# Kernel optimization log

Measured on AMD Instinct MI355X. Metric: run time of the kernel, lower is better.

## Reference

```python
import jax, jax.numpy as jnp
import numpy as np

B, S = 512, 256          # batch, seq_len
C, H = 8, 16             # num_cells, expert hidden size
M = 20                   # memory_size (hard-coded in module)
NT = C * H               # num_trajectories = 128
ENC_IN = M * (NT + 1)    # 20*129 = 2580, memory_encode input dim
A_H = 16                 # agent LSTM hidden


def setup_inputs() -> dict:
    key = jax.random.key(0)
    ks = jax.random.split(key, 20)
    r = lambda i, shape: 0.1 * jax.random.normal(ks[i], shape, dtype=jnp.float32)
    return {
        "x": jax.random.normal(ks[0], (B, S, 1), dtype=jnp.float32),
        "pred0": jax.random.uniform(ks[1], (B, 1), dtype=jnp.float32),
        "gate0": jax.nn.softmax(jax.random.uniform(ks[2], (B, C), dtype=jnp.float32), axis=1),
        # experts: C parallel LSTM cells (input 1, hidden H) + per-cell scalar head
        "W_ih": r(3, (C, 4 * H, 1)), "W_hh": r(4, (C, 4 * H, H)),
        "b_ih": r(5, (C, 4 * H)), "b_hh": r(6, (C, 4 * H)),
        "W_o": r(7, (C, H)), "b_o": r(8, (C,)),
        # memory_encode: Linear(2580,64) ReLU Linear(64,16) ReLU
        "W1": r(9, (64, ENC_IN)), "b1": r(10, (64,)),
        "W2": r(11, (16, 64)), "b2": r(12, (16,)),
        # gate_linear: Linear(16, C) + softmax
        "Wg": r(13, (C, 16)), "bg": r(14, (C,)),
        # agent: 2 stacked LSTM cells (16 -> 16)
        "Wa_ih": r(15, (2, 4 * A_H, A_H)), "Wa_hh": r(16, (2, 4 * A_H, A_H)),
        "ba_ih": r(17, (2, 4 * A_H)), "ba_hh": r(18, (2, 4 * A_H)),
    }


def _cell(z, c):
    # PyTorch LSTMCell gate order: i, f, g, o
    i, f, g, o = jnp.split(z, 4, axis=-1)
    c2 = jax.nn.sigmoid(f) * c + jax.nn.sigmoid(i) * jnp.tanh(g)
    return jax.nn.sigmoid(o) * jnp.tanh(c2), c2


def reference(x, pred0, gate0, W_ih, W_hh, b_ih, b_hh, W_o, b_o,
              W1, b1, W2, b2, Wg, bg, Wa_ih, Wa_hh, ba_ih, ba_hh):
    mem0 = jnp.zeros((B, M, NT + 1), jnp.float32).at[:, :, -1].set(0.5)
    eh0 = jnp.zeros((B, H), jnp.float32)   # combined expert h (shared across cells)
    a0 = jnp.zeros((2, B, A_H), jnp.float32)

    def step(carry, x_t):
        mem, eh, ec, pred, gate_state, ah, ac = carry
        error = x_t - pred                                        # [B,1]
        # experts: C LSTM cells, all reading the shared combined state
        z = (jnp.einsum('bf,cgf->bcg', x_t, W_ih)
             + jnp.einsum('bh,cgh->bcg', eh, W_hh)
             + b_ih + b_hh)                                       # [B,C,4H]
        nh, nc = _cell(z, ec[:, None, :])                          # [B,C,H]
        o = jnp.einsum('bch,ch->bc', nh, W_o) + b_o               # [B,C]
        # memory_step: matmul(mstep, mem) shifts rows down by 1, row 0 <- w
        w = jnp.concatenate([nh.reshape(B, -1), error], axis=1)   # [B,NT+1]
        mem = jnp.concatenate([w[:, None, :], mem[:, :-1, :]], axis=1)
        # memory_encode MLP
        e1 = jax.nn.relu(mem.reshape(B, -1) @ W1.T + b1)
        ai = jax.nn.relu(e1 @ W2.T + b2)                           # [B,16]
        # agent: 2 stacked LSTM cells
        ah_l, ac_l, inp_l = [], [], ai
        for l in range(2):
            zl = inp_l @ Wa_ih[l].T + ba_ih[l] + ah[l] @ Wa_hh[l].T + ba_hh[l]
            hl, cl = _cell(zl, ac[l])
            ah_l.append(hl); ac_l.append(cl)
            inp_l = hl
        ah2, ac2 = jnp.stack(ah_l), jnp.stack(ac_l)
        gate = jax.nn.softmax(inp_l @ Wg.T + bg, axis=1)           # [B,C]
        # theta = clip(2.5 * mean|mem[:, :10, -1]|, 0, 1)  (relu(t)-relu(t-1))
        theta = jnp.clip(jnp.mean(jnp.abs(mem[:, :10, -1]), axis=1) * 2.5, 0.0, 1.0)[:, None]
        gate = gate * theta + gate_state * (1.0 - theta)
        eh2 = jnp.einsum('bc,bch->bh', gate, nh)                   # bmm(gate, h)
        ec2 = jnp.einsum('bc,bch->bh', gate, nc)
        pred2 = jnp.einsum('bc,bc->b', gate, o)[:, None]           # [B,1]
        return (mem, eh2, ec2, pred2, gate, ah2, ac2), pred2

    xs = jnp.swapaxes(x, 0, 1)  # [S,B,1]
    _, preds = jax.lax.scan(step, (mem0, eh0, eh0, pred0, gate0, a0, a0), xs)
    return jnp.swapaxes(preds, 0, 1)  # [B,S,1]
```

## Files before the change

### kernel.cpp

```cpp
#include <hip/hip_runtime.h>
#include <math.h>

#define S_LEN 256
#define NCELL 8
#define HID 16
#define MEM 20
#define NB 4
#define NTHR 512
#define RSTR 2592

typedef _Float16 v8h __attribute__((ext_vector_type(8)));
typedef float v4f __attribute__((ext_vector_type(4)));

__device__ __forceinline__ float sigm(float v) { return 1.0f / (1.0f + __expf(-v)); }
__device__ __forceinline__ float tanh_f(float v) { return 1.0f - 2.0f / (__expf(2.0f * v) + 1.0f); }
__device__ __forceinline__ float dot4(float4 a, float4 b) {
    return fmaf(a.x, b.x, fmaf(a.y, b.y, fmaf(a.z, b.z, a.w * b.w)));
}
__device__ __forceinline__ v4f mfma16(v8h a, v8h b, v4f c) {
    return __builtin_amdgcn_mfma_f32_16x16x32_f16(a, b, c, 0, 0, 0);
}

#define RING(b, s, k) ringH[(b) * RSTR + (s) * 128 + (k)]

__global__ __launch_bounds__(256)
void prep_w1(const float* __restrict__ W1, _Float16* __restrict__ W1F) {
    int idx = blockIdx.x * 256 + threadIdx.x;
    if (idx < MEM * 4 * 4 * 64 * 8) {
        int e = idx & 7;
        int lane = (idx >> 3) & 63;
        int jt = (idx >> 9) & 3;
        int t = idx >> 11;
        int m = t >> 2, kc = t & 3;
        int j = jt * 16 + (lane & 15);
        int k = kc * 32 + (lane >> 4) * 8 + e;
        W1F[idx] = (_Float16)W1[j * 2580 + m * 129 + k];
    }
}

#define E1P(BB, V) { \
    V = b1_l[lane] \
      + red[par][1][BB][lane] + red[par][2][BB][lane] + red[par][3][BB][lane] \
      + red[par][4][BB][lane] + red[par][5][BB][lane] + red[par][6][BB][lane] \
      + red[par][7][BB][lane]; }

#define E1F(BB, V) { \
    V += errdotS[BB][lane] \
       + red0[0][BB][lane] + red0[1][BB][lane] + red0[2][BB][lane] + red0[3][BB][lane]; \
    e1S[BB][lane] = fmaxf(V, 0.f); }

__global__ __attribute__((amdgpu_flat_work_group_size(NTHR, NTHR)))
void mmoe_kernel(const float* __restrict__ x, const float* __restrict__ pred0,
                 const float* __restrict__ gate0,
                 const float* __restrict__ W_ih, const float* __restrict__ W_hh,
                 const float* __restrict__ b_ih, const float* __restrict__ b_hh,
                 const float* __restrict__ W_o, const float* __restrict__ b_o,
                 const float* __restrict__ W1, const float* __restrict__ b1,
                 const float* __restrict__ W2, const float* __restrict__ b2,
                 const float* __restrict__ Wg, const float* __restrict__ bg,
                 const float* __restrict__ Wa_ih, const float* __restrict__ Wa_hh,
                 const float* __restrict__ ba_ih, const float* __restrict__ ba_hh,
                 const _Float16* __restrict__ W1F,
                 float* __restrict__ out)
{
    __shared__ __align__(16) _Float16 ringH[NB * RSTR];
    __shared__ __align__(16) _Float16 W10F_l[8192];
    __shared__ float errS[NB][MEM];
    __shared__ __align__(16) float Whh_l[512 * 20];
    __shared__ float Wih_l[512], bias_l[512];
    __shared__ __align__(16) float WaI[2][64 * 20], WaH[2][64 * 20];
    __shared__ float ba_l[2][64];
    __shared__ __align__(16) float W2_l[16 * 68];
    __shared__ float b2_l[16];
    __shared__ __align__(16) float Wg_l[8][16], Wo_l[8][16];
    __shared__ float bg_l[8], bo_l[8];
    __shared__ float Werr_l[MEM * 64];
    __shared__ float b1_l[64];
    __shared__ float xS[NB][S_LEN];
    __shared__ __align__(16) float ehS[NB][HID], ecS[NB][HID];
    __shared__ __align__(16) float nhS[NB][NCELL][HID], ncS[NB][NCELL][HID];
    __shared__ float oS[NB][NCELL], predS[NB], gateS[NB][NCELL];
    __shared__ __align__(16) float ahS[2][NB][HID], acS[2][NB][HID];
    __shared__ __align__(16) float e1S[NB][64], aiS[NB][HID];
    __shared__ __align__(16) float glog[NB][8];
    __shared__ __align__(16) float red[2][8][NB][64];
    __shared__ __align__(16) float red0[4][NB][64];
    __shared__ float errdotS[NB][64];
    __shared__ float thS[NB];

    const int tid = threadIdx.x;
    const int b0 = blockIdx.x * NB;
    const int lane = tid & 63, wv = tid >> 6;
    const int quad = lane >> 4, nn = lane & 15, bb4 = nn & 3;

    for (int i = tid; i < 512 * 16; i += NTHR) { int g = i >> 4, q = i & 15; Whh_l[g * 20 + q] = W_hh[i]; }
    for (int i = tid; i < 512; i += NTHR) { Wih_l[i] = W_ih[i]; bias_l[i] = b_ih[i] + b_hh[i]; }
    for (int i = tid; i < 2048; i += NTHR) {
        int l = i >> 10, r = i & 1023, g = r >> 4, q = r & 15;
        WaI[l][g * 20 + q] = Wa_ih[i]; WaH[l][g * 20 + q] = Wa_hh[i];
    }
    for (int i = tid; i < 128; i += NTHR) { int l = i >> 6, g = i & 63; ba_l[l][g] = ba_ih[i] + ba_hh[i]; }
    for (int i = tid; i < 1024; i += NTHR) { int r = i >> 6, q = i & 63; W2_l[r * 68 + q] = W2[i]; }
    for (int i = tid; i < 1280; i += NTHR) { int m = i >> 6, j = i & 63; Werr_l[i] = W1[j * 2580 + m * 129 + 128]; }
    for (int i = tid; i < 8192; i += NTHR) W10F_l[i] = W1F[i];
    if (tid < 64) b1_l[tid] = b1[tid];
    if (tid < 16) b2_l[tid] = b2[tid];
    if (tid < 128) { int c = tid >> 4, h = tid & 15; Wg_l[c][h] = Wg[tid]; Wo_l[c][h] = W_o[tid]; }
    if (tid < 8) { bg_l[tid] = bg[tid]; bo_l[tid] = b_o[tid]; }
    for (int i = tid; i < NB * S_LEN; i += NTHR) { int b = i >> 8, s = i & 255; xS[b][s] = x[(b0 + b) * S_LEN + s]; }
    for (int i = tid; i < NB * RSTR; i += NTHR) ringH[i] = (_Float16)0.0f;
    for (int i = tid; i < 2 * 8 * NB * 64; i += NTHR) ((float*)red)[i] = 0.0f;
    if (tid < NB * MEM) { int b = tid / MEM, m = tid % MEM; errS[b][m] = 0.5f; }
    if (tid < NB * HID) {
        int b = tid >> 4, h = tid & 15;
        ehS[b][h] = 0.f; ecS[b][h] = 0.f;
        ahS[0][b][h] = 0.f; ahS[1][b][h] = 0.f;
        acS[0][b][h] = 0.f; acS[1][b][h] = 0.f;
    }
    if (tid < NB) predS[tid] = pred0[b0 + tid];
    if (tid < NB * NCELL) { int b = tid >> 3, c = tid & 7; gateS[b][c] = gate0[(b0 + b) * NCELL + c]; }
    __syncthreads();

    const v8h* Wb = (const v8h*)W1F;
    const v8h* WL = (const v8h*)W10F_l;

    int head = 0;
    #pragma unroll 1
    for (int t = 0; t < S_LEN; ++t) {
        head = (head == 0) ? (MEM - 1) : (head - 1);
        const int par = t & 1, np = par ^ 1;
        float v0, v1, v2, v3;

        {
            int b = tid >> 7, c = (tid >> 4) & 7, h = tid & 15;
            float xv = xS[b][t];
            const float4* ep = (const float4*)&ehS[b][0];
            float4 e0 = ep[0], e1v = ep[1], e2 = ep[2], e3 = ep[3];
            float zg[4];
            #pragma unroll
            for (int gi = 0; gi < 4; ++gi) {
                int g = c * 64 + gi * 16 + h;
                const float* wr = &Whh_l[g * 20];
                float z = bias_l[g] + xv * Wih_l[g];
                z += dot4(e0, *(const float4*)&wr[0]) + dot4(e1v, *(const float4*)&wr[4])
                   + dot4(e2, *(const float4*)&wr[8]) + dot4(e3, *(const float4*)&wr[12]);
                zg[gi] = z;
            }
            float cc = ecS[b][h];
            float c2 = sigm(zg[1]) * cc + sigm(zg[0]) * tanh_f(zg[2]);
            float hv = sigm(zg[3]) * tanh_f(c2);
            nhS[b][c][h] = hv; ncS[b][c][h] = c2;
            RING(b, head, c * 16 + h) = (_Float16)hv;
            if (tid < NB) errS[tid][head] = xS[tid][t] - predS[tid];
        }
        __syncthreads();

        {
            int kc = wv >> 1, jt0 = (wv & 1) * 2;
            v8h bfrag = *(const v8h*)&RING(bb4, head, kc * 32 + quad * 8);
            v8h a0 = WL[(kc * 4 + jt0) * 64 + lane];
            v8h a1 = WL[(kc * 4 + jt0 + 1) * 64 + lane];
            v4f z = {0.f, 0.f, 0.f, 0.f};
            v4f c0 = mfma16(a0, bfrag, z);
            v4f c1 = mfma16(a1, bfrag, z);
            if (nn < 4) {
                *(v4f*)&red0[kc][nn][jt0 * 16 + quad * 4] = c0;
                *(v4f*)&red0[kc][nn][(jt0 + 1) * 16 + quad * 4] = c1;
            }
            if (wv == 0) {
                E1P(0, v0) E1P(1, v1) E1P(2, v2) E1P(3, v3)
            } else if (wv == 1) {
                if (lane < 32) {
                    int bb = lane >> 3, c = lane & 7;
                    const float4* np_ = (const float4*)&nhS[bb][c][0];
                    const float4* wp = (const float4*)&Wo_l[c][0];
                    float s = bo_l[c];
                    #pragma unroll
                    for (int q4 = 0; q4 < 4; ++q4) s += dot4(np_[q4], wp[q4]);
                    oS[bb][c] = s;
                }
            } else if (wv == 2) {
                if (lane < NB) {
                    float th = 0.f;
                    #pragma unroll
                    for (int m = 0; m < 10; ++m) {
                        int sl = head + m; if (sl >= MEM) sl -= MEM;
                        th += fabsf(errS[lane][sl]);
                    }
                    th *= 0.25f;
                    thS[lane] = fminf(fmaxf(th, 0.f), 1.f);
                }
            } else if (wv >= 3 && wv < 7) {
                int bb = wv - 3;
                float s = 0.f;
                int sl = head;
                #pragma unroll
                for (int m = 0; m < MEM; ++m) {
                    s = fmaf(Werr_l[m * 64 + lane], errS[bb][sl], s);
                    ++sl; if (sl >= MEM) sl = 0;
                }
                errdotS[bb][lane] = s;
            }
        }
        __syncthreads();

        if (wv >= 1) {
            int kt = (wv - 1) * 11;
            int ktEnd = kt + 11; if (ktEnd > 76) ktEnd = 76;
            v4f c0 = {0.f,0.f,0.f,0.f}, c1 = {0.f,0.f,0.f,0.f};
            v4f c2 = {0.f,0.f,0.f,0.f}, c3 = {0.f,0.f,0.f,0.f};
            size_t t0 = (size_t)(4 + kt) * 256 + lane;
            v8h aA0 = Wb[t0], aA1 = Wb[t0 + 64], aA2 = Wb[t0 + 128], aA3 = Wb[t0 + 192];
            int m0 = 1 + (kt >> 2), kc0 = kt & 3;
            int s0 = head + m0 - 1; if (s0 >= MEM) s0 -= MEM;
            v8h aB = *(const v8h*)&RING(bb4, s0, kc0 * 32 + quad * 8);
            size_t t1 = t0 + 256;
            v8h bA0 = Wb[t1], bA1 = Wb[t1 + 64], bA2 = Wb[t1 + 128], bA3 = Wb[t1 + 192];
            int k1 = kt + 1, m1 = 1 + (k1 >> 2), kc1 = k1 & 3;
            int s1 = head + m1 - 1; if (s1 >= MEM) s1 -= MEM;
            v8h bB = *(const v8h*)&RING(bb4, s1, kc1 * 32 + quad * 8);
            #pragma unroll 1
            for (int i = kt; i < ktEnd; ++i) {
                v8h uA0 = aA0, uA1 = aA1, uA2 = aA2, uA3 = aA3, uB = aB;
                aA0 = bA0; aA1 = bA1; aA2 = bA2; aA3 = bA3; aB = bB;
                int kn = i + 2;
                if (kn < ktEnd) {
                    size_t tn = (size_t)(4 + kn) * 256 + lane;
                    bA0 = Wb[tn]; bA1 = Wb[tn + 64]; bA2 = Wb[tn + 128]; bA3 = Wb[tn + 192];
                    int mn = 1 + (kn >> 2), kcn = kn & 3;
                    int sn = head + mn - 1; if (sn >= MEM) sn -= MEM;
                    bB = *(const v8h*)&RING(bb4, sn, kcn * 32 + quad * 8);
                }
                c0 = mfma16(uA0, uB, c0);
                c1 = mfma16(uA1, uB, c1);
                c2 = mfma16(uA2, uB, c2);
                c3 = mfma16(uA3, uB, c3);
            }
            if (nn < 4) {
                *(v4f*)&red[np][wv][nn][ 0 + quad * 4] = c0;
                *(v4f*)&red[np][wv][nn][16 + quad * 4] = c1;
                *(v4f*)&red[np][wv][nn][32 + quad * 4] = c2;
                *(v4f*)&red[np][wv][nn][48 + quad * 4] = c3;
            }
        } else {
            E1F(0, v0) E1F(1, v1) E1F(2, v2) E1F(3, v3)
            const int j = lane;
            {
                int bb = j >> 4, i = j & 15;
                const float4* epq = (const float4*)&e1S[bb][0];
                float s = b2_l[i];
                #pragma unroll
                for (int q = 0; q < 16; ++q) s += dot4(*(const float4*)&W2_l[i * 68 + q * 4], epq[q]);
                aiS[bb][i] = fmaxf(s, 0.f);
            }
            #pragma unroll
            for (int l = 0; l < 2; ++l) {
                int bb = j >> 4, h = j & 15;
                const float4* ip = (l == 0) ? (const float4*)&aiS[bb][0]
                                            : (const float4*)&ahS[0][bb][0];
                const float4* hp = (const float4*)&ahS[l][bb][0];
                float4 i0 = ip[0], i1 = ip[1], i2 = ip[2], i3 = ip[3];
                float4 h0 = hp[0], h1 = hp[1], h2v = hp[2], h3 = hp[3];
                float zg[4];
                #pragma unroll
                for (int gi = 0; gi < 4; ++gi) {
                    int g = gi * 16 + h;
                    const float* wi = &WaI[l][g * 20];
                    const float* wh = &WaH[l][g * 20];
                    float z = ba_l[l][g];
                    z += dot4(i0, *(const float4*)&wi[0]) + dot4(i1, *(const float4*)&wi[4])
                       + dot4(i2, *(const float4*)&wi[8]) + dot4(i3, *(const float4*)&wi[12]);
                    z += dot4(h0, *(const float4*)&wh[0]) + dot4(h1, *(const float4*)&wh[4])
                       + dot4(h2v, *(const float4*)&wh[8]) + dot4(h3, *(const float4*)&wh[12]);
                    zg[gi] = z;
                }
                float c2 = sigm(zg[1]) * acS[l][bb][h] + sigm(zg[0]) * tanh_f(zg[2]);
                acS[l][bb][h] = c2;
                ahS[l][bb][h] = sigm(zg[3]) * tanh_f(c2);
            }
            if (j < 32) {
                int bb = j >> 3, c = j & 7;
                const float4* hp = (const float4*)&ahS[1][bb][0];
                const float4* wg = (const float4*)&Wg_l[c][0];
                float s = bg_l[c];
                #pragma unroll
                for (int q = 0; q < 4; ++q) s += dot4(wg[q], hp[q]);
                glog[bb][c] = s;
                float4 ga = *(const float4*)&glog[bb][0];
                float4 gb = *(const float4*)&glog[bb][4];
                float mx = fmaxf(fmaxf(fmaxf(ga.x, ga.y), fmaxf(ga.z, ga.w)),
                                 fmaxf(fmaxf(gb.x, gb.y), fmaxf(gb.z, gb.w)));
                float sum = __expf(ga.x - mx) + __expf(ga.y - mx) + __expf(ga.z - mx) + __expf(ga.w - mx)
                          + __expf(gb.x - mx) + __expf(gb.y - mx) + __expf(gb.z - mx) + __expf(gb.w - mx);
                float p = __expf(s - mx) / sum;
                float th = thS[bb];
                gateS[bb][c] = p * th + gateS[bb][c] * (1.f - th);
            }
            {
                int bb = j >> 4, h = j & 15;
                float se = 0.f, sc = 0.f;
                #pragma unroll
                for (int c = 0; c < 8; ++c) {
                    float g = gateS[bb][c];
                    se = fmaf(g, nhS[bb][c][h], se);
                    sc = fmaf(g, ncS[bb][c][h], sc);
                }
                ehS[bb][h] = se; ecS[bb][h] = sc;
            }
            if (j < NB) {
                float s = 0.f;
                #pragma unroll
                for (int c = 0; c < 8; ++c) s = fmaf(gateS[j][c], oS[j][c], s);
                predS[j] = s;
                out[(b0 + j) * S_LEN + t] = s;
            }
        }
        __syncthreads();
    }
}

extern "C" void kernel_launch(void* const* d_in, const int* in_sizes, int n_in,
                              void* d_out, int out_size, void* d_ws, size_t ws_size,
                              hipStream_t stream) {
    const float* xp    = (const float*)d_in[0];
    const float* pred0 = (const float*)d_in[1];
    const float* gate0 = (const float*)d_in[2];
    const float* W_ih  = (const float*)d_in[3];
    const float* W_hh  = (const float*)d_in[4];
    const float* b_ih  = (const float*)d_in[5];
    const float* b_hh  = (const float*)d_in[6];
    const float* W_o   = (const float*)d_in[7];
    const float* b_o   = (const float*)d_in[8];
    const float* W1    = (const float*)d_in[9];
    const float* b1    = (const float*)d_in[10];
    const float* W2    = (const float*)d_in[11];
    const float* b2    = (const float*)d_in[12];
    const float* Wg    = (const float*)d_in[13];
    const float* bg    = (const float*)d_in[14];
    const float* Wa_ih = (const float*)d_in[15];
    const float* Wa_hh = (const float*)d_in[16];
    const float* ba_ih = (const float*)d_in[17];
    const float* ba_hh = (const float*)d_in[18];
    _Float16* W1F = (_Float16*)d_ws;

    prep_w1<<<(MEM * 4 * 4 * 64 * 8 + 255) / 256, 256, 0, stream>>>(W1, W1F);
    mmoe_kernel<<<512 / NB, NTHR, 0, stream>>>(
        xp, pred0, gate0, W_ih, W_hh, b_ih, b_hh, W_o, b_o,
        W1, b1, W2, b2, Wg, bg, Wa_ih, Wa_hh, ba_ih, ba_hh,
        W1F, (float*)d_out);
}
```

Baseline: 1.333 ms.

## Compute expert LSTM gates with fp16 MFMA instead of scalar dot products

Moves the per-step expert LSTM gate computation (8 cells x 64 gates x 16 inputs plus input weight and bias) onto 16x16x32 fp16 MFMA. The weights, input weight and bias are packed into register-resident A fragments, and the combined hidden state, current x and a constant 1 are kept in an fp16 shared vector that serves as the B operand. This removes the large fp32 W_hh shared-memory table and the scalar dot loops. It also shortens the W1 software pipeline from two stages of prefetch to one. The cost is fp16 rounding of the recurrent state, x and biases, which may reduce accuracy, and only a quarter of the lanes now do the gate nonlinearity work.

Result: no change. 1.314 ms (-1.4%).

```diff
diff --git a/kernel.cpp b/kernel.cpp
--- a/kernel.cpp
+++ b/kernel.cpp
@@ -24,17 +24,27 @@
 #define RING(b, s, k) ringH[(b) * RSTR + (s) * 128 + (k)]
 
 __global__ __launch_bounds__(256)
-void prep_w1(const float* __restrict__ W1, _Float16* __restrict__ W1F) {
+void prep_w(const float* __restrict__ W1, const float* __restrict__ W_hh,
+            const float* __restrict__ W_ih, const float* __restrict__ b_ih,
+            const float* __restrict__ b_hh, _Float16* __restrict__ W1F,
+            _Float16* __restrict__ WAF) {
     int idx = blockIdx.x * 256 + threadIdx.x;
-    if (idx < MEM * 4 * 4 * 64 * 8) {
-        int e = idx & 7;
-        int lane = (idx >> 3) & 63;
-        int jt = (idx >> 9) & 3;
-        int t = idx >> 11;
+    if (idx < 163840) {
+        int e = idx & 7, lane = (idx >> 3) & 63, jt = (idx >> 9) & 3, t = idx >> 11;
         int m = t >> 2, kc = t & 3;
         int j = jt * 16 + (lane & 15);
         int k = kc * 32 + (lane >> 4) * 8 + e;
         W1F[idx] = (_Float16)W1[j * 2580 + m * 129 + k];
+    } else if (idx < 163840 + 16384) {
+        int d = idx - 163840;
+        int e = d & 7, lane = (d >> 3) & 63, gate = (d >> 9) & 3, c = d >> 11;
+        int m = lane & 15, k = (lane >> 4) * 8 + e;
+        int row = c * 64 + gate * 16 + m;
+        float v = 0.f;
+        if (k < 16) v = W_hh[row * 16 + k];
+        else if (k == 16) v = W_ih[row];
+        else if (k == 17) v = b_ih[row] + b_hh[row];
+        WAF[d] = (_Float16)v;
     }
 }
 
@@ -60,14 +70,13 @@
                  const float* __restrict__ Wg, const float* __restrict__ bg,
                  const float* __restrict__ Wa_ih, const float* __restrict__ Wa_hh,
                  const float* __restrict__ ba_ih, const float* __restrict__ ba_hh,
-                 const _Float16* __restrict__ W1F,
+                 const _Float16* __restrict__ W1F, const _Float16* __restrict__ WAF,
                  float* __restrict__ out)
 {
     __shared__ __align__(16) _Float16 ringH[NB * RSTR];
     __shared__ __align__(16) _Float16 W10F_l[8192];
+    __shared__ __align__(16) _Float16 ehH[NB][40];
     __shared__ float errS[NB][MEM];
-    __shared__ __align__(16) float Whh_l[512 * 20];
-    __shared__ float Wih_l[512], bias_l[512];
     __shared__ __align__(16) float WaI[2][64 * 20], WaH[2][64 * 20];
     __shared__ float ba_l[2][64];
     __shared__ __align__(16) float W2_l[16 * 68];
@@ -77,7 +86,7 @@
     __shared__ float Werr_l[MEM * 64];
     __shared__ float b1_l[64];
     __shared__ float xS[NB][S_LEN];
-    __shared__ __align__(16) float ehS[NB][HID], ecS[NB][HID];
+    __shared__ __align__(16) float ecS[NB][HID];
     __shared__ __align__(16) float nhS[NB][NCELL][HID], ncS[NB][NCELL][HID];
     __shared__ float oS[NB][NCELL], predS[NB], gateS[NB][NCELL];
     __shared__ __align__(16) float ahS[2][NB][HID], acS[2][NB][HID];
@@ -93,8 +102,6 @@
     const int lane = tid & 63, wv = tid >> 6;
     const int quad = lane >> 4, nn = lane & 15, bb4 = nn & 3;
 
-    for (int i = tid; i < 512 * 16; i += NTHR) { int g = i >> 4, q = i & 15; Whh_l[g * 20 + q] = W_hh[i]; }
-    for (int i = tid; i < 512; i += NTHR) { Wih_l[i] = W_ih[i]; bias_l[i] = b_ih[i] + b_hh[i]; }
     for (int i = tid; i < 2048; i += NTHR) {
         int l = i >> 10, r = i & 1023, g = r >> 4, q = r & 15;
         WaI[l][g * 20 + q] = Wa_ih[i]; WaH[l][g * 20 + q] = Wa_hh[i];
@@ -110,15 +117,28 @@
     for (int i = tid; i < NB * S_LEN; i += NTHR) { int b = i >> 8, s = i & 255; xS[b][s] = x[(b0 + b) * S_LEN + s]; }
     for (int i = tid; i < NB * RSTR; i += NTHR) ringH[i] = (_Float16)0.0f;
     for (int i = tid; i < 2 * 8 * NB * 64; i += NTHR) ((float*)red)[i] = 0.0f;
+    if (tid < NB * 40) {
+        int n = tid / 40, k = tid % 40;
+        float v = 0.f;
+        if (k == 16) v = x[(b0 + n) * S_LEN + 0];
+        else if (k == 17) v = 1.0f;
+        ehH[n][k] = (_Float16)v;
+    }
     if (tid < NB * MEM) { int b = tid / MEM, m = tid % MEM; errS[b][m] = 0.5f; }
     if (tid < NB * HID) {
         int b = tid >> 4, h = tid & 15;
-        ehS[b][h] = 0.f; ecS[b][h] = 0.f;
+        ecS[b][h] = 0.f;
         ahS[0][b][h] = 0.f; ahS[1][b][h] = 0.f;
         acS[0][b][h] = 0.f; acS[1][b][h] = 0.f;
     }
     if (tid < NB) predS[tid] = pred0[b0 + tid];
     if (tid < NB * NCELL) { int b = tid >> 3, c = tid & 7; gateS[b][c] = gate0[(b0 + b) * NCELL + c]; }
+
+    const v8h* WA = (const v8h*)WAF;
+    v8h aI = WA[(wv * 4 + 0) * 64 + lane];
+    v8h aF = WA[(wv * 4 + 1) * 64 + lane];
+    v8h aG = WA[(wv * 4 + 2) * 64 + lane];
+    v8h aO = WA[(wv * 4 + 3) * 64 + lane];
     __syncthreads();
 
     const v8h* Wb = (const v8h*)W1F;
@@ -132,25 +152,24 @@
         float v0, v1, v2, v3;
 
         {
-            int b = tid >> 7, c = (tid >> 4) & 7, h = tid & 15;
-            float xv = xS[b][t];
-            const float4* ep = (const float4*)&ehS[b][0];
-            float4 e0 = ep[0], e1v = ep[1], e2 = ep[2], e3 = ep[3];
-            float zg[4];
-            #pragma unroll
-            for (int gi = 0; gi < 4; ++gi) {
-                int g = c * 64 + gi * 16 + h;
-                const float* wr = &Whh_l[g * 20];
-                float z = bias_l[g] + xv * Wih_l[g];
-                z += dot4(e0, *(const float4*)&wr[0]) + dot4(e1v, *(const float4*)&wr[4])
-                   + dot4(e2, *(const float4*)&wr[8]) + dot4(e3, *(const float4*)&wr[12]);
-                zg[gi] = z;
-            }
-            float cc = ecS[b][h];
-            float c2 = sigm(zg[1]) * cc + sigm(zg[0]) * tanh_f(zg[2]);
-            float hv = sigm(zg[3]) * tanh_f(c2);
-            nhS[b][c][h] = hv; ncS[b][c][h] = c2;
-            RING(b, head, c * 16 + h) = (_Float16)hv;
+            v8h bfrag = *(const v8h*)&ehH[bb4][quad * 8];
+            v4f z4 = {0.f, 0.f, 0.f, 0.f};
+            v4f zi = mfma16(aI, bfrag, z4);
+            v4f zf = mfma16(aF, bfrag, z4);
+            v4f zg = mfma16(aG, bfrag, z4);
+            v4f zo = mfma16(aO, bfrag, z4);
+            if (nn < 4) {
+                int b = nn, c = wv;
+                #pragma unroll
+                for (int r = 0; r < 4; ++r) {
+                    int h = quad * 4 + r;
+                    float cc = ecS[b][h];
+                    float c2 = sigm(zf[r]) * cc + sigm(zi[r]) * tanh_f(zg[r]);
+                    float hv = sigm(zo[r]) * tanh_f(c2);
+                    nhS[b][c][h] = hv; ncS[b][c][h] = c2;
+                    RING(b, head, c * 16 + h) = (_Float16)hv;
+                }
+            }
             if (tid < NB) errS[tid][head] = xS[tid][t] - predS[tid];
         }
         __syncthreads();
@@ -209,32 +228,26 @@
             int ktEnd = kt + 11; if (ktEnd > 76) ktEnd = 76;
             v4f c0 = {0.f,0.f,0.f,0.f}, c1 = {0.f,0.f,0.f,0.f};
             v4f c2 = {0.f,0.f,0.f,0.f}, c3 = {0.f,0.f,0.f,0.f};
-            size_t t0 = (size_t)(4 + kt) * 256 + lane;
-            v8h aA0 = Wb[t0], aA1 = Wb[t0 + 64], aA2 = Wb[t0 + 128], aA3 = Wb[t0 + 192];
+            size_t tb = (size_t)(4 + kt) * 256 + lane;
+            v8h pA0 = Wb[tb], pA1 = Wb[tb + 64], pA2 = Wb[tb + 128], pA3 = Wb[tb + 192];
             int m0 = 1 + (kt >> 2), kc0 = kt & 3;
             int s0 = head + m0 - 1; if (s0 >= MEM) s0 -= MEM;
-            v8h aB = *(const v8h*)&RING(bb4, s0, kc0 * 32 + quad * 8);
-            size_t t1 = t0 + 256;
-            v8h bA0 = Wb[t1], bA1 = Wb[t1 + 64], bA2 = Wb[t1 + 128], bA3 = Wb[t1 + 192];
-            int k1 = kt + 1, m1 = 1 + (k1 >> 2), kc1 = k1 & 3;
-            int s1 = head + m1 - 1; if (s1 >= MEM) s1 -= MEM;
-            v8h bB = *(const v8h*)&RING(bb4, s1, kc1 * 32 + quad * 8);
+            v8h pB = *(const v8h*)&RING(bb4, s0, kc0 * 32 + quad * 8);
             #pragma unroll 1
-            for (int i = kt; i < ktEnd; ++i) {
-                v8h uA0 = aA0, uA1 = aA1, uA2 = aA2, uA3 = aA3, uB = aB;
-                aA0 = bA0; aA1 = bA1; aA2 = bA2; aA3 = bA3; aB = bB;
-                int kn = i + 2;
+            for (; kt < ktEnd; ++kt) {
+                v8h A0 = pA0, A1 = pA1, A2 = pA2, A3 = pA3, B = pB;
+                int kn = kt + 1;
                 if (kn < ktEnd) {
                     size_t tn = (size_t)(4 + kn) * 256 + lane;
-                    bA0 = Wb[tn]; bA1 = Wb[tn + 64]; bA2 = Wb[tn + 128]; bA3 = Wb[tn + 192];
+                    pA0 = Wb[tn]; pA1 = Wb[tn + 64]; pA2 = Wb[tn + 128]; pA3 = Wb[tn + 192];
                     int mn = 1 + (kn >> 2), kcn = kn & 3;
                     int sn = head + mn - 1; if (sn >= MEM) sn -= MEM;
-                    bB = *(const v8h*)&RING(bb4, sn, kcn * 32 + quad * 8);
-                }
-                c0 = mfma16(uA0, uB, c0);
-                c1 = mfma16(uA1, uB, c1);
-                c2 = mfma16(uA2, uB, c2);
-                c3 = mfma16(uA3, uB, c3);
+                    pB = *(const v8h*)&RING(bb4, sn, kcn * 32 + quad * 8);
+                }
+                c0 = mfma16(A0, B, c0);
+                c1 = mfma16(A1, B, c1);
+                c2 = mfma16(A2, B, c2);
+                c3 = mfma16(A3, B, c3);
             }
             if (nn < 4) {
                 *(v4f*)&red[np][wv][nn][ 0 + quad * 4] = c0;
@@ -305,7 +318,8 @@
                     se = fmaf(g, nhS[bb][c][h], se);
                     sc = fmaf(g, ncS[bb][c][h], sc);
                 }
-                ehS[bb][h] = se; ecS[bb][h] = sc;
+                ehH[bb][h] = (_Float16)se;
+                ecS[bb][h] = sc;
             }
             if (j < NB) {
                 float s = 0.f;
@@ -313,6 +327,7 @@
                 for (int c = 0; c < 8; ++c) s = fmaf(gateS[j][c], oS[j][c], s);
                 predS[j] = s;
                 out[(b0 + j) * S_LEN + t] = s;
+                ehH[j][16] = (_Float16)((t + 1 < S_LEN) ? xS[j][t + 1] : 0.f);
             }
         }
         __syncthreads();
@@ -342,10 +357,12 @@
     const float* ba_ih = (const float*)d_in[17];
     const float* ba_hh = (const float*)d_in[18];
     _Float16* W1F = (_Float16*)d_ws;
-
-    prep_w1<<<(MEM * 4 * 4 * 64 * 8 + 255) / 256, 256, 0, stream>>>(W1, W1F);
+    _Float16* WAF = W1F + 163840;
+
+    prep_w<<<(163840 + 16384 + 255) / 256, 256, 0, stream>>>(
+        W1, W_hh, W_ih, b_ih, b_hh, W1F, WAF);
     mmoe_kernel<<<512 / NB, NTHR, 0, stream>>>(
         xp, pred0, gate0, W_ih, W_hh, b_ih, b_hh, W_o, b_o,
         W1, b1, W2, b2, Wg, bg, Wa_ih, Wa_hh, ba_ih, ba_hh,
-        W1F, (float*)d_out);
-}
+        W1F, WAF, (float*)d_out);
+}
```
